# Performance work log

Measured on AMD Instinct MI355X. Metric: run time of the kernel, lower is better.

Reference implementation:

```python
import jax, jax.numpy as jnp
import numpy as np

HIDDEN = 2048
NUM_HEADS = 8
NUM_KV_HEADS = 1
HEAD_DIM = 256
ROPE_THETA = 10000.0
B, S = 2, 2048


def setup_inputs() -> dict:
    key = jax.random.key(0)
    k1, k2, k3, k4, k5 = jax.random.split(key, 5)
    scale = 0.02
    hidden_states = jax.random.normal(k1, (B, S, HIDDEN), dtype=jnp.float32)
    Wq = jax.random.normal(k2, (HIDDEN, NUM_HEADS * HEAD_DIM), dtype=jnp.float32) * scale
    Wk = jax.random.normal(k3, (HIDDEN, NUM_KV_HEADS * HEAD_DIM), dtype=jnp.float32) * scale
    Wv = jax.random.normal(k4, (HIDDEN, NUM_KV_HEADS * HEAD_DIM), dtype=jnp.float32) * scale
    Wo = jax.random.normal(k5, (NUM_HEADS * HEAD_DIM, HIDDEN), dtype=jnp.float32) * scale
    # causal mask: 1 = attend, 0 = masked (module adds -1e9 where mask==0)
    attention_mask = jnp.tril(jnp.ones((S, S), dtype=jnp.int32))[None, None].repeat(B, axis=0)
    position_ids = jnp.arange(S, dtype=jnp.int32)[None, :].repeat(B, axis=0)
    return {"hidden_states": hidden_states, "Wq": Wq, "Wk": Wk, "Wv": Wv,
            "Wo": Wo, "attention_mask": attention_mask, "position_ids": position_ids}


def _rotate_half(x):
    half = x.shape[-1] // 2
    return jnp.concatenate([-x[..., half:], x[..., :half]], axis=-1)


def _rope_cos_sin(position_ids, head_dim, theta):
    inv_freq = 1.0 / (theta ** (jnp.arange(0, head_dim, 2, dtype=jnp.float32) / head_dim))
    freqs = position_ids.astype(jnp.float32)[:, :, None] * inv_freq[None, None, :]  # [B,S,D/2]
    emb = jnp.concatenate([freqs, freqs], axis=-1)  # [B,S,D]
    return jnp.cos(emb)[:, None], jnp.sin(emb)[:, None]  # [B,1,S,D]


def reference(hidden_states, Wq, Wk, Wv, Wo, attention_mask, position_ids):
    bsz, q_len, _ = hidden_states.shape
    q = (hidden_states @ Wq).reshape(bsz, q_len, NUM_HEADS, HEAD_DIM).transpose(0, 2, 1, 3)
    k = (hidden_states @ Wk).reshape(bsz, q_len, NUM_KV_HEADS, HEAD_DIM).transpose(0, 2, 1, 3)
    v = (hidden_states @ Wv).reshape(bsz, q_len, NUM_KV_HEADS, HEAD_DIM).transpose(0, 2, 1, 3)
    q = q / jnp.sqrt(jnp.float32(HEAD_DIM))  # scale before RoPE, as in source
    cos, sin = _rope_cos_sin(position_ids, HEAD_DIM, ROPE_THETA)
    q = q * cos + _rotate_half(q) * sin
    k = k * cos + _rotate_half(k) * sin
    # GQA: repeat kv heads (prefill: cache == current k,v)
    groups = NUM_HEADS // NUM_KV_HEADS
    k = jnp.repeat(k, groups, axis=1)
    v = jnp.repeat(v, groups, axis=1)
    attn = jnp.einsum('bhqd,bhkd->bhqk', q, k)  # [B,H,S,S]
    additive = jnp.where(attention_mask == 0, jnp.float32(-1e9), jnp.float32(0.0))
    attn = jax.nn.softmax(attn + additive, axis=-1)
    out = jnp.einsum('bhqk,bhkd->bhqd', attn, v)
    out = out.transpose(0, 2, 1, 3).reshape(bsz, q_len, NUM_HEADS * HEAD_DIM)
    out = out @ Wo
    return out, attn
```

## Files before the change

### kernel.cpp

```cpp
#include <hip/hip_runtime.h>

typedef __bf16 bf16_t;
typedef __attribute__((ext_vector_type(4))) float f32x4;
typedef __attribute__((ext_vector_type(8))) __bf16 bf16x8;
typedef __attribute__((ext_vector_type(4))) __bf16 bf16x4;

#define DEVI __device__ __forceinline__

static constexpr int kBsz = 2, kS = 2048, kH = 8, kD = 256, kHid = 2048, kNqkv = 2560;

DEVI void gload_lds16(const void* g, void* l) {
  __builtin_amdgcn_global_load_lds(
      (__attribute__((address_space(1))) unsigned int*)g,
      (__attribute__((address_space(3))) unsigned int*)l, 16, 0, 0);
}

__global__ __launch_bounds__(256) void cast_f32_bf16(const float* __restrict__ in,
                                                     bf16_t* __restrict__ out) {
  int idx = blockIdx.x * 256 + threadIdx.x;
  const float4 f = ((const float4*)in)[idx];
  bf16x4 o;
  o[0] = (bf16_t)f.x; o[1] = (bf16_t)f.y; o[2] = (bf16_t)f.z; o[3] = (bf16_t)f.w;
  ((bf16x4*)out)[idx] = o;
}

__global__ __launch_bounds__(256) void transpose_cast(const float* __restrict__ in,
                                                      bf16_t* __restrict__ out,
                                                      int R, int C) {
  __shared__ float tile[32][33];
  int c0 = blockIdx.x * 32, r0 = blockIdx.y * 32;
  int tx = threadIdx.x, ty = threadIdx.y;
#pragma unroll
  for (int k = 0; k < 4; k++)
    tile[ty + 8 * k][tx] = in[(size_t)(r0 + ty + 8 * k) * C + c0 + tx];
  __syncthreads();
#pragma unroll
  for (int k = 0; k < 4; k++)
    out[(size_t)(c0 + ty + 8 * k) * R + r0 + tx] = (bf16_t)tile[tx][ty + 8 * k];
}

__global__ __launch_bounds__(256) void transpose_v(const float* __restrict__ qkv,
                                                   bf16_t* __restrict__ vT) {
  __shared__ float tile[32][33];
  int d0 = blockIdx.x * 32, s0 = blockIdx.y * 32, b = blockIdx.z;
  int tx = threadIdx.x, ty = threadIdx.y;
  const float* in = qkv + ((size_t)(b * kS + s0)) * kNqkv + 2304 + d0;
#pragma unroll
  for (int k = 0; k < 4; k++)
    tile[ty + 8 * k][tx] = in[(size_t)(ty + 8 * k) * kNqkv + tx];
  __syncthreads();
  bf16_t* out = vT + ((size_t)(b * kD + d0)) * kS + s0;
#pragma unroll
  for (int k = 0; k < 4; k++)
    out[(size_t)(ty + 8 * k) * kS + tx] = (bf16_t)tile[tx][ty + 8 * k];
}

__global__ __launch_bounds__(256) void rope_q(const float* __restrict__ qkv,
                                              const int* __restrict__ pos_ids,
                                              bf16_t* __restrict__ q_bh) {
  int idx = blockIdx.x * 256 + threadIdx.x;
  int j = idx & 127;
  int s = (idx >> 7) & 2047;
  int h = (idx >> 18) & 7;
  int b = idx >> 21;
  float invf = exp2f(-0.103810253f * (float)j);
  float pos = (float)pos_ids[b * kS + s];
  float ang = pos * invf;
  float c, sn;
  sincosf(ang, &sn, &c);
  const float* src = qkv + ((size_t)(b * kS + s)) * kNqkv + h * kD;
  float x0 = src[j] * 0.0625f;
  float x1 = src[j + 128] * 0.0625f;
  bf16_t* dst = q_bh + ((size_t)((b * kH + h) * kS + s)) * kD;
  dst[j] = (bf16_t)(x0 * c - x1 * sn);
  dst[j + 128] = (bf16_t)(x1 * c + x0 * sn);
}

__global__ __launch_bounds__(256) void rope_k(const float* __restrict__ qkv,
                                              const int* __restrict__ pos_ids,
                                              bf16_t* __restrict__ k_b) {
  int idx = blockIdx.x * 256 + threadIdx.x;
  int j = idx & 127;
  int s = (idx >> 7) & 2047;
  int b = idx >> 18;
  float invf = exp2f(-0.103810253f * (float)j);
  float pos = (float)pos_ids[b * kS + s];
  float ang = pos * invf;
  float c, sn;
  sincosf(ang, &sn, &c);
  const float* src = qkv + ((size_t)(b * kS + s)) * kNqkv + 2048;
  float x0 = src[j];
  float x1 = src[j + 128];
  bf16_t* dst = k_b + ((size_t)(b * kS + s)) * kD;
  dst[j] = (bf16_t)(x0 * c - x1 * sn);
  dst[j + 128] = (bf16_t)(x1 * c + x0 * sn);
}

__global__ __launch_bounds__(256) void softmax_causal(float* __restrict__ attn) {
  int rowid = blockIdx.x;
  int i = rowid & (kS - 1);
  float* r = attn + (size_t)rowid * kS;
  int L = i + 1;
  int t = threadIdx.x;
  int nIt = (L + 255) >> 8;
  float rv[8];
  float mx = -1e30f;
#pragma unroll
  for (int it = 0; it < 8; it++) {
    if (it >= nIt) break;
    int j = (it << 8) + t;
    rv[it] = (j < L) ? r[j] : -1e30f;
    mx = fmaxf(mx, rv[it]);
  }
  __shared__ float redm[4], reds[4];
#pragma unroll
  for (int o = 32; o > 0; o >>= 1) mx = fmaxf(mx, __shfl_down(mx, o));
  if ((t & 63) == 0) redm[t >> 6] = mx;
  __syncthreads();
  mx = fmaxf(fmaxf(redm[0], redm[1]), fmaxf(redm[2], redm[3]));
  float sm = 0.f;
#pragma unroll
  for (int it = 0; it < 8; it++) {
    if (it >= nIt) break;
    float e = expf(rv[it] - mx);
    rv[it] = e;
    sm += e;
  }
#pragma unroll
  for (int o = 32; o > 0; o >>= 1) sm += __shfl_down(sm, o);
  if ((t & 63) == 0) reds[t >> 6] = sm;
  __syncthreads();
  sm = reds[0] + reds[1] + reds[2] + reds[3];
  float inv = 1.f / sm;
#pragma unroll
  for (int it = 0; it < 8; it++) {
    if (it >= nIt) break;
    int j = (it << 8) + t;
    if (j < L) r[j] = rv[it] * inv;
  }
  for (int j = L + t; j < kS; j += 256) r[j] = 0.f;
}

template <int AF32, int OUTAV, int CSKIP, int CKTR>
__global__ __launch_bounds__(256) void gemm_bt(
    const void* __restrict__ Av, const bf16_t* __restrict__ Btv, void* __restrict__ Cv,
    int K, int lda, int ldb, int ldc,
    long long aBatch, long long bBatch, int bzShift, long long cBatch) {
  constexpr int BM = 128, BN = 128, BK = 32;
  __shared__ bf16_t As[BM * BK];
  __shared__ bf16_t Bs[BN * BK];
  const int z = blockIdx.z;
  const int n0 = blockIdx.x * BN;
  const int m0 = blockIdx.y * BM;
  if (CSKIP && n0 >= m0 + BM) return;
  const bf16_t* Bt = Btv + (size_t)(z >> bzShift) * bBatch + (size_t)n0 * ldb;
  const int kEnd = CKTR ? ((m0 + BM < K) ? (m0 + BM) : K) : K;
  const int t = threadIdx.x;
  const int lane = t & 63, wv = t >> 6;
  const int wm = (wv & 1) << 6, wn = (wv >> 1) << 6;
  const int lrow = lane & 15, quad = lane >> 4;
  f32x4 zero = {0.f, 0.f, 0.f, 0.f};
  f32x4 acc[4][4];
#pragma unroll
  for (int i = 0; i < 4; i++)
#pragma unroll
    for (int j = 0; j < 4; j++) acc[i][j] = zero;

  const bf16_t* Ab = nullptr;
  const float* Af = nullptr;
  if (AF32)
    Af = (const float*)Av + (size_t)z * aBatch + (size_t)m0 * lda;
  else
    Ab = (const bf16_t*)Av + (size_t)z * aBatch + (size_t)m0 * lda;

  for (int k0 = 0; k0 < kEnd; k0 += BK) {
    __syncthreads();
    if (!AF32) {
      const bf16_t* ga = Ab + (size_t)(t >> 2) * lda + k0 + (t & 3) * 8;
      gload_lds16(ga, As + t * 8);
      gload_lds16(ga + (size_t)64 * lda, As + 2048 + t * 8);
    } else {
      const int arow = t >> 1, acol = (t & 1) * 16;
      const float* ga = Af + (size_t)arow * lda + k0 + acol;
      float4 f0 = *(const float4*)(ga);
      float4 f1 = *(const float4*)(ga + 4);
      float4 f2 = *(const float4*)(ga + 8);
      float4 f3 = *(const float4*)(ga + 12);
      bf16x8 lo, hi;
      lo[0] = (bf16_t)f0.x; lo[1] = (bf16_t)f0.y; lo[2] = (bf16_t)f0.z; lo[3] = (bf16_t)f0.w;
      lo[4] = (bf16_t)f1.x; lo[5] = (bf16_t)f1.y; lo[6] = (bf16_t)f1.z; lo[7] = (bf16_t)f1.w;
      hi[0] = (bf16_t)f2.x; hi[1] = (bf16_t)f2.y; hi[2] = (bf16_t)f2.z; hi[3] = (bf16_t)f2.w;
      hi[4] = (bf16_t)f3.x; hi[5] = (bf16_t)f3.y; hi[6] = (bf16_t)f3.z; hi[7] = (bf16_t)f3.w;
      *(bf16x8*)(As + arow * 32 + acol) = lo;
      *(bf16x8*)(As + arow * 32 + acol + 8) = hi;
    }
    {
      const bf16_t* gb = Bt + (size_t)(t >> 2) * ldb + k0 + (t & 3) * 8;
      gload_lds16(gb, Bs + t * 8);
      gload_lds16(gb + (size_t)64 * ldb, Bs + 2048 + t * 8);
    }
    __syncthreads();
    bf16x8 af[4], bfv[4];
#pragma unroll
    for (int i = 0; i < 4; i++)
      af[i] = *(const bf16x8*)(As + (wm + i * 16 + lrow) * BK + quad * 8);
#pragma unroll
    for (int i = 0; i < 4; i++)
      bfv[i] = *(const bf16x8*)(Bs + (wn + i * 16 + lrow) * BK + quad * 8);
#pragma unroll
    for (int mi = 0; mi < 4; mi++)
#pragma unroll
      for (int ni = 0; ni < 4; ni++)
        acc[mi][ni] = __builtin_amdgcn_mfma_f32_16x16x32_bf16(af[mi], bfv[ni], acc[mi][ni], 0, 0, 0);
  }

  if (!OUTAV) {
    float* C = (float*)Cv + (size_t)z * cBatch;
#pragma unroll
    for (int mi = 0; mi < 4; mi++) {
      int m = m0 + wm + mi * 16 + quad * 4;
#pragma unroll
      for (int ni = 0; ni < 4; ni++) {
        int n = n0 + wn + ni * 16 + lrow;
#pragma unroll
        for (int r = 0; r < 4; r++) C[(size_t)(m + r) * ldc + n] = acc[mi][ni][r];
      }
    }
  } else {
    bf16_t* C = (bf16_t*)Cv + (size_t)(z >> 3) * cBatch + (size_t)(z & 7) * kD;
#pragma unroll
    for (int mi = 0; mi < 4; mi++) {
      int m = m0 + wm + mi * 16 + quad * 4;
#pragma unroll
      for (int ni = 0; ni < 4; ni++) {
        int n = n0 + wn + ni * 16 + lrow;
#pragma unroll
        for (int r = 0; r < 4; r++) C[(size_t)(m + r) * ldc + n] = (bf16_t)acc[mi][ni][r];
      }
    }
  }
}

extern "C" void kernel_launch(void* const* d_in, const int* in_sizes, int n_in,
                              void* d_out, int out_size, void* d_ws, size_t ws_size,
                              hipStream_t stream) {
  const float* hs = (const float*)d_in[0];
  const float* Wq = (const float*)d_in[1];
  const float* Wk = (const float*)d_in[2];
  const float* Wv = (const float*)d_in[3];
  const float* Wo = (const float*)d_in[4];
  const int* pos = (const int*)d_in[6];

  float* out = (float*)d_out;
  float* attn = out + (size_t)kBsz * kS * kHid;

  char* w = (char*)d_ws;
  bf16_t* hsb = (bf16_t*)w;      w += (size_t)4096 * 2048 * 2;
  bf16_t* WqkvT = (bf16_t*)w;    w += (size_t)2560 * 2048 * 2;
  bf16_t* WoT = (bf16_t*)w;      w += (size_t)2048 * 2048 * 2;
  float* qkv = (float*)w;        w += (size_t)4096 * 2560 * 4;
  bf16_t* q_bh = (bf16_t*)w;     w += (size_t)8388608 * 2;
  bf16_t* k_b = (bf16_t*)w;      w += (size_t)1048576 * 2;
  bf16_t* vT = (bf16_t*)w;       w += (size_t)1048576 * 2;
  bf16_t* av = (bf16_t*)w;       w += (size_t)8388608 * 2;

  cast_f32_bf16<<<8192, 256, 0, stream>>>(hs, hsb);
  transpose_cast<<<dim3(64, 64), dim3(32, 8), 0, stream>>>(Wq, WqkvT, 2048, 2048);
  transpose_cast<<<dim3(8, 64), dim3(32, 8), 0, stream>>>(Wk, WqkvT + (size_t)2048 * 2048, 2048, 256);
  transpose_cast<<<dim3(8, 64), dim3(32, 8), 0, stream>>>(Wv, WqkvT + (size_t)2304 * 2048, 2048, 256);
  transpose_cast<<<dim3(64, 64), dim3(32, 8), 0, stream>>>(Wo, WoT, 2048, 2048);

  gemm_bt<0, 0, 0, 0><<<dim3(20, 32, 1), 256, 0, stream>>>(
      hsb, WqkvT, qkv, 2048, 2048, 2048, 2560, 0, 0, 0, 0);

  rope_q<<<16384, 256, 0, stream>>>(qkv, pos, q_bh);
  rope_k<<<2048, 256, 0, stream>>>(qkv, pos, k_b);
  transpose_v<<<dim3(8, 64, 2), dim3(32, 8), 0, stream>>>(qkv, vT);

  gemm_bt<0, 0, 1, 0><<<dim3(16, 16, 16), 256, 0, stream>>>(
      q_bh, k_b, attn, 256, 256, 256, 2048,
      (long long)524288, (long long)524288, 3, (long long)4194304);

  softmax_causal<<<32768, 256, 0, stream>>>(attn);

  gemm_bt<1, 1, 0, 1><<<dim3(2, 16, 16), 256, 0, stream>>>(
      attn, vT, av, 2048, 2048, 2048, 2048,
      (long long)4194304, (long long)524288, 3, (long long)(kS * kHid));

  gemm_bt<0, 0, 0, 0><<<dim3(16, 32, 1), 256, 0, stream>>>(
      av, WoT, out, 2048, 2048, 2048, 2048, 0, 0, 0, 0);
}
```

Measured before the change: 725.1 us.

## Store QKV projection in bf16 and feed PV GEMM a bf16 probability copy

After: 716.7 us. No clear change (-1.2%).

```diff
diff --git a/kernel.cpp b/kernel.cpp
--- a/kernel.cpp
+++ b/kernel.cpp
@@ -39,15 +39,15 @@
     out[(size_t)(c0 + ty + 8 * k) * R + r0 + tx] = (bf16_t)tile[tx][ty + 8 * k];
 }
 
-__global__ __launch_bounds__(256) void transpose_v(const float* __restrict__ qkv,
+__global__ __launch_bounds__(256) void transpose_v(const bf16_t* __restrict__ qkv,
                                                    bf16_t* __restrict__ vT) {
   __shared__ float tile[32][33];
   int d0 = blockIdx.x * 32, s0 = blockIdx.y * 32, b = blockIdx.z;
   int tx = threadIdx.x, ty = threadIdx.y;
-  const float* in = qkv + ((size_t)(b * kS + s0)) * kNqkv + 2304 + d0;
-#pragma unroll
-  for (int k = 0; k < 4; k++)
-    tile[ty + 8 * k][tx] = in[(size_t)(ty + 8 * k) * kNqkv + tx];
+  const bf16_t* in = qkv + ((size_t)(b * kS + s0)) * kNqkv + 2304 + d0;
+#pragma unroll
+  for (int k = 0; k < 4; k++)
+    tile[ty + 8 * k][tx] = (float)in[(size_t)(ty + 8 * k) * kNqkv + tx];
   __syncthreads();
   bf16_t* out = vT + ((size_t)(b * kD + d0)) * kS + s0;
 #pragma unroll
@@ -55,7 +55,7 @@
     out[(size_t)(ty + 8 * k) * kS + tx] = (bf16_t)tile[tx][ty + 8 * k];
 }
 
-__global__ __launch_bounds__(256) void rope_q(const float* __restrict__ qkv,
+__global__ __launch_bounds__(256) void rope_q(const bf16_t* __restrict__ qkv,
                                               const int* __restrict__ pos_ids,
                                               bf16_t* __restrict__ q_bh) {
   int idx = blockIdx.x * 256 + threadIdx.x;
@@ -68,15 +68,15 @@
   float ang = pos * invf;
   float c, sn;
   sincosf(ang, &sn, &c);
-  const float* src = qkv + ((size_t)(b * kS + s)) * kNqkv + h * kD;
-  float x0 = src[j] * 0.0625f;
-  float x1 = src[j + 128] * 0.0625f;
+  const bf16_t* src = qkv + ((size_t)(b * kS + s)) * kNqkv + h * kD;
+  float x0 = (float)src[j] * 0.0625f;
+  float x1 = (float)src[j + 128] * 0.0625f;
   bf16_t* dst = q_bh + ((size_t)((b * kH + h) * kS + s)) * kD;
   dst[j] = (bf16_t)(x0 * c - x1 * sn);
   dst[j + 128] = (bf16_t)(x1 * c + x0 * sn);
 }
 
-__global__ __launch_bounds__(256) void rope_k(const float* __restrict__ qkv,
+__global__ __launch_bounds__(256) void rope_k(const bf16_t* __restrict__ qkv,
                                               const int* __restrict__ pos_ids,
                                               bf16_t* __restrict__ k_b) {
   int idx = blockIdx.x * 256 + threadIdx.x;
@@ -88,19 +88,22 @@
   float ang = pos * invf;
   float c, sn;
   sincosf(ang, &sn, &c);
-  const float* src = qkv + ((size_t)(b * kS + s)) * kNqkv + 2048;
-  float x0 = src[j];
-  float x1 = src[j + 128];
+  const bf16_t* src = qkv + ((size_t)(b * kS + s)) * kNqkv + 2048;
+  float x0 = (float)src[j];
+  float x1 = (float)src[j + 128];
   bf16_t* dst = k_b + ((size_t)(b * kS + s)) * kD;
   dst[j] = (bf16_t)(x0 * c - x1 * sn);
   dst[j + 128] = (bf16_t)(x1 * c + x0 * sn);
 }
 
-__global__ __launch_bounds__(256) void softmax_causal(float* __restrict__ attn) {
+__global__ __launch_bounds__(256) void softmax_causal(float* __restrict__ attn,
+                                                      bf16_t* __restrict__ P) {
   int rowid = blockIdx.x;
   int i = rowid & (kS - 1);
   float* r = attn + (size_t)rowid * kS;
+  bf16_t* p = P + (size_t)rowid * kS;
   int L = i + 1;
+  int padEnd = ((i >> 7) + 1) << 7;
   int t = threadIdx.x;
   int nIt = (L + 255) >> 8;
   float rv[8];
@@ -136,14 +139,19 @@
   for (int it = 0; it < 8; it++) {
     if (it >= nIt) break;
     int j = (it << 8) + t;
-    if (j < L) r[j] = rv[it] * inv;
+    if (j < L) {
+      float v = rv[it] * inv;
+      r[j] = v;
+      p[j] = (bf16_t)v;
+    }
   }
   for (int j = L + t; j < kS; j += 256) r[j] = 0.f;
-}
-
-template <int AF32, int OUTAV, int CSKIP, int CKTR>
+  for (int j = L + t; j < padEnd; j += 256) p[j] = (bf16_t)0.f;
+}
+
+template <int OUT, int CSKIP, int CKTR>
 __global__ __launch_bounds__(256) void gemm_bt(
-    const void* __restrict__ Av, const bf16_t* __restrict__ Btv, void* __restrict__ Cv,
+    const bf16_t* __restrict__ Av, const bf16_t* __restrict__ Btv, void* __restrict__ Cv,
     int K, int lda, int ldb, int ldc,
     long long aBatch, long long bBatch, int bzShift, long long cBatch) {
   constexpr int BM = 128, BN = 128, BK = 32;
@@ -166,33 +174,14 @@
 #pragma unroll
     for (int j = 0; j < 4; j++) acc[i][j] = zero;
 
-  const bf16_t* Ab = nullptr;
-  const float* Af = nullptr;
-  if (AF32)
-    Af = (const float*)Av + (size_t)z * aBatch + (size_t)m0 * lda;
-  else
-    Ab = (const bf16_t*)Av + (size_t)z * aBatch + (size_t)m0 * lda;
+  const bf16_t* Ab = Av + (size_t)z * aBatch + (size_t)m0 * lda;
 
   for (int k0 = 0; k0 < kEnd; k0 += BK) {
     __syncthreads();
-    if (!AF32) {
+    {
       const bf16_t* ga = Ab + (size_t)(t >> 2) * lda + k0 + (t & 3) * 8;
       gload_lds16(ga, As + t * 8);
       gload_lds16(ga + (size_t)64 * lda, As + 2048 + t * 8);
-    } else {
-      const int arow = t >> 1, acol = (t & 1) * 16;
-      const float* ga = Af + (size_t)arow * lda + k0 + acol;
-      float4 f0 = *(const float4*)(ga);
-      float4 f1 = *(const float4*)(ga + 4);
-      float4 f2 = *(const float4*)(ga + 8);
-      float4 f3 = *(const float4*)(ga + 12);
-      bf16x8 lo, hi;
-      lo[0] = (bf16_t)f0.x; lo[1] = (bf16_t)f0.y; lo[2] = (bf16_t)f0.z; lo[3] = (bf16_t)f0.w;
-      lo[4] = (bf16_t)f1.x; lo[5] = (bf16_t)f1.y; lo[6] = (bf16_t)f1.z; lo[7] = (bf16_t)f1.w;
-      hi[0] = (bf16_t)f2.x; hi[1] = (bf16_t)f2.y; hi[2] = (bf16_t)f2.z; hi[3] = (bf16_t)f2.w;
-      hi[4] = (bf16_t)f3.x; hi[5] = (bf16_t)f3.y; hi[6] = (bf16_t)f3.z; hi[7] = (bf16_t)f3.w;
-      *(bf16x8*)(As + arow * 32 + acol) = lo;
-      *(bf16x8*)(As + arow * 32 + acol + 8) = hi;
     }
     {
       const bf16_t* gb = Bt + (size_t)(t >> 2) * ldb + k0 + (t & 3) * 8;
@@ -214,7 +203,7 @@
         acc[mi][ni] = __builtin_amdgcn_mfma_f32_16x16x32_bf16(af[mi], bfv[ni], acc[mi][ni], 0, 0, 0);
   }
 
-  if (!OUTAV) {
+  if (OUT == 0) {
     float* C = (float*)Cv + (size_t)z * cBatch;
 #pragma unroll
     for (int mi = 0; mi < 4; mi++) {
@@ -226,8 +215,20 @@
         for (int r = 0; r < 4; r++) C[(size_t)(m + r) * ldc + n] = acc[mi][ni][r];
       }
     }
+  } else if (OUT == 1) {
+    bf16_t* C = (bf16_t*)Cv + (size_t)(z >> 3) * cBatch + (size_t)(z & 7) * kD;
+#pragma unroll
+    for (int mi = 0; mi < 4; mi++) {
+      int m = m0 + wm + mi * 16 + quad * 4;
+#pragma unroll
+      for (int ni = 0; ni < 4; ni++) {
+        int n = n0 + wn + ni * 16 + lrow;
+#pragma unroll
+        for (int r = 0; r < 4; r++) C[(size_t)(m + r) * ldc + n] = (bf16_t)acc[mi][ni][r];
+      }
+    }
   } else {
-    bf16_t* C = (bf16_t*)Cv + (size_t)(z >> 3) * cBatch + (size_t)(z & 7) * kD;
+    bf16_t* C = (bf16_t*)Cv + (size_t)z * cBatch;
 #pragma unroll
     for (int mi = 0; mi < 4; mi++) {
       int m = m0 + wm + mi * 16 + quad * 4;
@@ -258,11 +259,12 @@
   bf16_t* hsb = (bf16_t*)w;      w += (size_t)4096 * 2048 * 2;
   bf16_t* WqkvT = (bf16_t*)w;    w += (size_t)2560 * 2048 * 2;
   bf16_t* WoT = (bf16_t*)w;      w += (size_t)2048 * 2048 * 2;
-  float* qkv = (float*)w;        w += (size_t)4096 * 2560 * 4;
+  bf16_t* qkv = (bf16_t*)w;      w += (size_t)4096 * 2560 * 2;
   bf16_t* q_bh = (bf16_t*)w;     w += (size_t)8388608 * 2;
   bf16_t* k_b = (bf16_t*)w;      w += (size_t)1048576 * 2;
   bf16_t* vT = (bf16_t*)w;       w += (size_t)1048576 * 2;
   bf16_t* av = (bf16_t*)w;       w += (size_t)8388608 * 2;
+  bf16_t* Pb = (bf16_t*)w;       w += (size_t)16 * 2048 * 2048 * 2;
 
   cast_f32_bf16<<<8192, 256, 0, stream>>>(hs, hsb);
   transpose_cast<<<dim3(64, 64), dim3(32, 8), 0, stream>>>(Wq, WqkvT, 2048, 2048);
@@ -270,23 +272,23 @@
   transpose_cast<<<dim3(8, 64), dim3(32, 8), 0, stream>>>(Wv, WqkvT + (size_t)2304 * 2048, 2048, 256);
   transpose_cast<<<dim3(64, 64), dim3(32, 8), 0, stream>>>(Wo, WoT, 2048, 2048);
 
-  gemm_bt<0, 0, 0, 0><<<dim3(20, 32, 1), 256, 0, stream>>>(
+  gemm_bt<2, 0, 0><<<dim3(20, 32, 1), 256, 0, stream>>>(
       hsb, WqkvT, qkv, 2048, 2048, 2048, 2560, 0, 0, 0, 0);
 
   rope_q<<<16384, 256, 0, stream>>>(qkv, pos, q_bh);
   rope_k<<<2048, 256, 0, stream>>>(qkv, pos, k_b);
   transpose_v<<<dim3(8, 64, 2), dim3(32, 8), 0, stream>>>(qkv, vT);
 
-  gemm_bt<0, 0, 1, 0><<<dim3(16, 16, 16), 256, 0, stream>>>(
+  gemm_bt<0, 1, 0><<<dim3(16, 16, 16), 256, 0, stream>>>(
       q_bh, k_b, attn, 256, 256, 256, 2048,
       (long long)524288, (long long)524288, 3, (long long)4194304);
 
-  softmax_causal<<<32768, 256, 0, stream>>>(attn);
-
-  gemm_bt<1, 1, 0, 1><<<dim3(2, 16, 16), 256, 0, stream>>>(
-      attn, vT, av, 2048, 2048, 2048, 2048,
+  softmax_causal<<<32768, 256, 0, stream>>>(attn, Pb);
+
+  gemm_bt<1, 0, 1><<<dim3(2, 16, 16), 256, 0, stream>>>(
+      Pb, vT, av, 2048, 2048, 2048, 2048,
       (long long)4194304, (long long)524288, 3, (long long)(kS * kHid));
 
-  gemm_bt<0, 0, 0, 0><<<dim3(16, 32, 1), 256, 0, stream>>>(
+  gemm_bt<0, 0, 0><<<dim3(16, 32, 1), 256, 0, stream>>>(
       av, WoT, out, 2048, 2048, 2048, 2048, 0, 0, 0, 0);
 }
```
